# Performance work log

Measured on AMD Instinct MI355X. Metric: run time of the kernel, lower is better.

Reference implementation:

```python
import jax, jax.numpy as jnp
import numpy as np

RADIUS = (0.1, 0.1, 0.1)  # radius_x, radius_y, radius_z (cube half-widths)
NSAMPLE = 32


def setup_inputs() -> dict:
    key = jax.random.key(0)
    k1, k2, k3 = jax.random.split(key, 3)
    B, Nb, Mb, C = 4, 16384, 4096, 64
    xyz = jax.random.uniform(k1, (B * Nb, 3), dtype=jnp.float32)
    new_xyz = jax.random.uniform(k2, (B * Mb, 3), dtype=jnp.float32)
    features = jax.random.normal(k3, (B * Nb, C), dtype=jnp.float32)
    xyz_batch_cnt = jnp.full((B,), Nb, dtype=jnp.int32)
    new_xyz_batch_cnt = jnp.full((B,), Mb, dtype=jnp.int32)
    return {
        "xyz": xyz,
        "xyz_batch_cnt": xyz_batch_cnt,
        "new_xyz": new_xyz,
        "new_xyz_batch_cnt": new_xyz_batch_cnt,
        "features": features,
    }


def _cube_query(xyz_b, new_b, rx, ry, rz, nsample):
    # xyz_b: (B, Nb, 3); new_b: (B, Mb, 3)
    Nb = xyz_b.shape[1]

    def per_batch(args):
        pts, qs = args  # (Nb,3), (Mb,3)
        # cube membership test per axis (avoid stacking a (Mb,Nb,3) tensor)
        mask = (
            (jnp.abs(qs[:, None, 0] - pts[None, :, 0]) < rx)
            & (jnp.abs(qs[:, None, 1] - pts[None, :, 1]) < ry)
            & (jnp.abs(qs[:, None, 2] - pts[None, :, 2]) < rz)
        )  # (Mb, Nb)
        # CUDA kernel keeps the FIRST nsample neighbors in point order:
        # score favors in-cube points, tie-broken by smallest index.
        score = jnp.where(mask, -jnp.arange(Nb, dtype=jnp.float32), -jnp.inf)
        vals, idx_local = jax.lax.top_k(score, nsample)  # (Mb, nsample)
        valid = jnp.isfinite(vals)  # non_padding
        return idx_local, valid

    # process one batch at a time to bound the MbxNb intermediate
    idx_l, valid = jax.lax.map(per_batch, (xyz_b, new_b))
    return idx_l, valid


def reference(xyz, xyz_batch_cnt, new_xyz, new_xyz_batch_cnt, features):
    rx, ry, rz = RADIUS
    nsample = NSAMPLE
    B = xyz_batch_cnt.shape[0]
    N, M = xyz.shape[0], new_xyz.shape[0]
    Nb, Mb = N // B, M // B  # equal counts per batch (matches setup_inputs)

    xyz_b = xyz.reshape(B, Nb, 3)
    new_b = new_xyz.reshape(B, Mb, 3)

    idx_l, valid = _cube_query(xyz_b, new_b, rx, ry, rz, nsample)
    # local -> global flattened indices (batch offsets)
    offsets = (jnp.arange(B, dtype=idx_l.dtype) * Nb)[:, None, None]
    idx = (idx_l + offsets).reshape(M, nsample)
    valid = valid.reshape(M, nsample)
    # torch zeroes idx for empty/padding slots before gather
    idx = jnp.where(valid, idx, 0)

    non_padding = valid.astype(features.dtype)  # (M, nsample)
    grouped = features[idx]  # (M, nsample, C) gather
    # empty_ball_mask + padding_mask zeroing, fused into one multiply
    grouped = grouped * non_padding[..., None]
    grouped = jnp.transpose(grouped, (0, 2, 1))  # (M, C, nsample)
    num_non_padding = jnp.sum(non_padding, axis=-1)  # (M,)
    return grouped, num_non_padding
```

## Files before the change

kernel.cpp:

```cpp
#include <hip/hip_runtime.h>

#define NSAMPLE 32
#define RADI 0.1f
#define WPB 4
#define MARGIN 0.0002f

#define NCELL 4
#define NBLKA 3
#define SPAN  2
#define NBLK3 27
#define CAP   3072
#define NSEG  64

typedef float nat_f32x4 __attribute__((ext_vector_type(4)));

__device__ __forceinline__ int cell_of(float x) {
    int c = (int)(x * (float)NCELL);
    c = c < 0 ? 0 : c;
    return c > (NCELL - 1) ? (NCELL - 1) : c;
}

__global__ __launch_bounds__(256) void pack_xyz_kernel(
    const float* __restrict__ xyz, float4* __restrict__ xyz4, int N)
{
    const int i = blockIdx.x * blockDim.x + threadIdx.x;
    if (i < N) {
        float4 v;
        v.x = xyz[i * 3 + 0];
        v.y = xyz[i * 3 + 1];
        v.z = xyz[i * 3 + 2];
        v.w = 0.0f;
        xyz4[i] = v;
    }
}

__global__ __launch_bounds__(64 * WPB) void count_kernel(
    const float4* __restrict__ xyz4, const int* __restrict__ xyz_cnt,
    int* __restrict__ segcnt, int B)
{
    const int wave = threadIdx.x >> 6, lane = threadIdx.x & 63;
    const int gw = blockIdx.x * WPB + wave;
    if (gw >= B * NBLK3 * NSEG) return;
    const int seg = gw % NSEG;
    const int blk = (gw / NSEG) % NBLK3;
    const int b   = gw / (NSEG * NBLK3);
    const int bx = blk % NBLKA, by = (blk / NBLKA) % NBLKA, bz = blk / (NBLKA * NBLKA);

    int xstart = 0;
    for (int i = 0; i < b; ++i) xstart += xyz_cnt[i];
    const int nb = xyz_cnt[b];
    const int seglen = (nb + NSEG - 1) / NSEG;
    const int p0 = seg * seglen;
    const int p1 = min(p0 + seglen, nb);

    int cnt = 0;
    for (int base = p0; base < p1; base += 256) {
        #pragma unroll
        for (int k = 0; k < 4; ++k) {
            const int p = base + k * 64 + lane;
            bool hit = false;
            if (p < p1) {
                const float4 v = xyz4[xstart + p];
                hit = ((unsigned)(cell_of(v.x) - bx) < (unsigned)SPAN) &
                      ((unsigned)(cell_of(v.y) - by) < (unsigned)SPAN) &
                      ((unsigned)(cell_of(v.z) - bz) < (unsigned)SPAN);
            }
            cnt += (int)__popcll(__ballot(hit));
        }
    }
    if (lane == 0) segcnt[gw] = cnt;
}

__global__ __launch_bounds__(64 * WPB) void fill_kernel(
    const float4* __restrict__ xyz4, const int* __restrict__ xyz_cnt,
    const int* __restrict__ segcnt, float4* __restrict__ blk_pts,
    int* __restrict__ blkcnt, int B)
{
    const int wave = threadIdx.x >> 6, lane = threadIdx.x & 63;
    const int gw = blockIdx.x * WPB + wave;
    if (gw >= B * NBLK3 * NSEG) return;
    const int seg = gw % NSEG;
    const int blk = (gw / NSEG) % NBLK3;
    const int b   = gw / (NSEG * NBLK3);
    const int bx = blk % NBLKA, by = (blk / NBLKA) % NBLKA, bz = blk / (NBLKA * NBLKA);

    int xstart = 0;
    for (int i = 0; i < b; ++i) xstart += xyz_cnt[i];
    const int nb = xyz_cnt[b];
    const int seglen = (nb + NSEG - 1) / NSEG;
    const int p0 = seg * seglen;
    const int p1 = min(p0 + seglen, nb);

    const int bid = b * NBLK3 + blk;
    int off = 0;
    const int sbase = bid * NSEG;
    for (int s = 0; s < seg; ++s) off += segcnt[sbase + s];

    float4* __restrict__ dst = blk_pts + (size_t)bid * CAP;
    const unsigned long long lt = (1ull << lane) - 1ull;

    int cnt = 0;
    for (int base = p0; base < p1; base += 256) {
        #pragma unroll
        for (int k = 0; k < 4; ++k) {
            const int p = base + k * 64 + lane;
            bool hit = false;
            float4 v;
            if (p < p1) {
                v = xyz4[xstart + p];
                hit = ((unsigned)(cell_of(v.x) - bx) < (unsigned)SPAN) &
                      ((unsigned)(cell_of(v.y) - by) < (unsigned)SPAN) &
                      ((unsigned)(cell_of(v.z) - bz) < (unsigned)SPAN);
            }
            const unsigned long long m = __ballot(hit);
            if (hit) {
                const int slot = off + cnt + (int)__popcll(m & lt);
                if (slot < CAP) {
                    v.w = __int_as_float(xstart + p);
                    dst[slot] = v;
                }
            }
            cnt += (int)__popcll(m);
        }
    }
    if (seg == NSEG - 1 && lane == 0) blkcnt[bid] = off + cnt;
}

__global__ __launch_bounds__(64 * WPB, 8) void query_kernel(
    const float4* __restrict__ blk_pts,
    const int*    __restrict__ blkcnt,
    const float*  __restrict__ new_xyz,
    const int*    __restrict__ new_cnt,
    const float*  __restrict__ features,
    float* __restrict__ out_grouped,
    float* __restrict__ out_cnt,
    int B, int M, int C)
{
    const int wave = threadIdx.x >> 6;
    const int lane = threadIdx.x & 63;
    const int q = blockIdx.x * WPB + wave;
    if (q >= M) return;

    __shared__ int s_idx_all[WPB][NSAMPLE];
    int* __restrict__ s_idx = s_idx_all[wave];
    if (lane < NSAMPLE) s_idx[lane] = 0;

    int b = 0, qacc = 0;
    for (int i = 0; i < B; ++i) {
        const int qc = new_cnt[i];
        if (q < qacc + qc) { b = i; break; }
        qacc += qc;
    }

    const float qx = new_xyz[q * 3 + 0];
    const float qy = new_xyz[q * 3 + 1];
    const float qz = new_xyz[q * 3 + 2];

    const int bxq = min(max((int)floorf((qx - RADI - MARGIN) * (float)NCELL), 0), NBLKA - 1);
    const int byq = min(max((int)floorf((qy - RADI - MARGIN) * (float)NCELL), 0), NBLKA - 1);
    const int bzq = min(max((int)floorf((qz - RADI - MARGIN) * (float)NCELL), 0), NBLKA - 1);
    const int bid = b * NBLK3 + bxq + NBLKA * byq + NBLKA * NBLKA * bzq;

    int lcnt = blkcnt[bid];
    if (lcnt > CAP) lcnt = CAP;

    const float4* __restrict__ lp = blk_pts + (size_t)bid * CAP;
    const unsigned long long lt = (1ull << lane) - 1ull;

    int found = 0, base = 0;
    const int nfull = lcnt & ~255;

    auto test_group = [&](const float4& v, bool inb) {
        const float m3 = fmaxf(fmaxf(fabsf(qx - v.x), fabsf(qy - v.y)),
                               fabsf(qz - v.z));
        const bool c = inb & (m3 < RADI);
        const unsigned long long m = __ballot(c);
        if (c) {
            const int slot = found + (int)__popcll(m & lt);
            if (slot < NSAMPLE) s_idx[slot] = __float_as_int(v.w);
        }
        found += (int)__popcll(m);
    };

    if (nfull > 0) {
        float4 A[4], Bb[4];
        #pragma unroll
        for (int k = 0; k < 4; ++k) A[k] = lp[k * 64 + lane];

        while (true) {
            int nxt = base + 256;
            if (nxt < nfull) {
                #pragma unroll
                for (int k = 0; k < 4; ++k) Bb[k] = lp[nxt + k * 64 + lane];
            }
            #pragma unroll
            for (int k = 0; k < 4; ++k) {
                test_group(A[k], true);
                if (found >= NSAMPLE) break;
            }
            base = nxt;
            if (found >= NSAMPLE || base >= nfull) break;

            nxt = base + 256;
            if (nxt < nfull) {
                #pragma unroll
                for (int k = 0; k < 4; ++k) A[k] = lp[nxt + k * 64 + lane];
            }
            #pragma unroll
            for (int k = 0; k < 4; ++k) {
                test_group(Bb[k], true);
                if (found >= NSAMPLE) break;
            }
            base = nxt;
            if (found >= NSAMPLE || base >= nfull) break;
        }
    }
    while (found < NSAMPLE && base < lcnt) {
        #pragma unroll
        for (int k = 0; k < 4; ++k) {
            const int p = base + k * 64 + lane;
            const bool inb = (p < lcnt);
            const float4 v = lp[inb ? p : 0];
            test_group(v, inb);
        }
        base += 256;
    }
    if (found > NSAMPLE) found = NSAMPLE;

    asm volatile("s_waitcnt lgkmcnt(0)" ::: "memory");
    __builtin_amdgcn_sched_barrier(0);

    const int s0  = 4 * (lane & 7);
    const int chi = lane >> 3;
    const int r0 = s_idx[s0 + 0];
    const int r1 = s_idx[s0 + 1];
    const int r2 = s_idx[s0 + 2];
    const int r3 = s_idx[s0 + 3];
    const float k0 = (s0 + 0) < found ? 1.0f : 0.0f;
    const float k1 = (s0 + 1) < found ? 1.0f : 0.0f;
    const float k2 = (s0 + 2) < found ? 1.0f : 0.0f;
    const float k3 = (s0 + 3) < found ? 1.0f : 0.0f;

    const float* __restrict__ f0p = features + (size_t)r0 * C;
    const float* __restrict__ f1p = features + (size_t)r1 * C;
    const float* __restrict__ f2p = features + (size_t)r2 * C;
    const float* __restrict__ f3p = features + (size_t)r3 * C;

    float* __restrict__ og = out_grouped + (size_t)q * (C * NSAMPLE);
    #pragma unroll
    for (int k = 0; k < 8; ++k) {
        const int c = 8 * k + chi;
        nat_f32x4 v;
        v.x = f0p[c] * k0;
        v.y = f1p[c] * k1;
        v.z = f2p[c] * k2;
        v.w = f3p[c] * k3;
        __builtin_nontemporal_store(v,
            reinterpret_cast<nat_f32x4*>(og + (size_t)(k * 64 + lane) * 4));
    }
    if (lane == 0) out_cnt[q] = (float)found;
}

__global__ __launch_bounds__(64 * WPB, 8) void fallback_kernel(
    const float* __restrict__ xyz, const int* __restrict__ xyz_cnt,
    const float* __restrict__ new_xyz, const int* __restrict__ new_cnt,
    const float* __restrict__ features,
    float* __restrict__ out_grouped, float* __restrict__ out_cnt,
    int B, int M, int C)
{
    const int wave = threadIdx.x >> 6, lane = threadIdx.x & 63;
    const int q = blockIdx.x * WPB + wave;
    if (q >= M) return;

    __shared__ int s_idx_all[WPB][NSAMPLE];
    int* __restrict__ s_idx = s_idx_all[wave];
    if (lane < NSAMPLE) s_idx[lane] = 0;

    int b = 0, qacc = 0, xstart = 0;
    for (int i = 0; i < B; ++i) {
        const int qc = new_cnt[i];
        if (q < qacc + qc) { b = i; break; }
        qacc += qc; xstart += xyz_cnt[i];
    }
    const int nb = xyz_cnt[b];
    const float qx = new_xyz[q * 3 + 0], qy = new_xyz[q * 3 + 1], qz = new_xyz[q * 3 + 2];
    const float* __restrict__ xp = xyz + (size_t)xstart * 3;
    const unsigned long long lt = (1ull << lane) - 1ull;

    int found = 0;
    for (int base = 0; base < nb && found < NSAMPLE; base += 64) {
        const int p = base + lane;
        bool c = false;
        if (p < nb) {
            const float dx = qx - xp[p * 3 + 0];
            const float dy = qy - xp[p * 3 + 1];
            const float dz = qz - xp[p * 3 + 2];
            c = (fabsf(dx) < RADI) && (fabsf(dy) < RADI) && (fabsf(dz) < RADI);
        }
        const unsigned long long m = __ballot(c);
        if (c) {
            const int slot = found + (int)__popcll(m & lt);
            if (slot < NSAMPLE) s_idx[slot] = xstart + p;
        }
        found += (int)__popcll(m);
    }
    if (found > NSAMPLE) found = NSAMPLE;

    asm volatile("s_waitcnt lgkmcnt(0)" ::: "memory");
    __builtin_amdgcn_sched_barrier(0);

    const int s0 = 4 * (lane & 7), chi = lane >> 3;
    const int r0 = s_idx[s0 + 0], r1 = s_idx[s0 + 1], r2 = s_idx[s0 + 2], r3 = s_idx[s0 + 3];
    const float k0 = (s0 + 0) < found ? 1.0f : 0.0f;
    const float k1 = (s0 + 1) < found ? 1.0f : 0.0f;
    const float k2 = (s0 + 2) < found ? 1.0f : 0.0f;
    const float k3 = (s0 + 3) < found ? 1.0f : 0.0f;
    const float* f0p = features + (size_t)r0 * C;
    const float* f1p = features + (size_t)r1 * C;
    const float* f2p = features + (size_t)r2 * C;
    const float* f3p = features + (size_t)r3 * C;
    float* __restrict__ og = out_grouped + (size_t)q * (C * NSAMPLE);
    #pragma unroll
    for (int k = 0; k < 8; ++k) {
        const int c = 8 * k + chi;
        float4 v;
        v.x = f0p[c] * k0; v.y = f1p[c] * k1; v.z = f2p[c] * k2; v.w = f3p[c] * k3;
        *reinterpret_cast<float4*>(og + (size_t)(k * 64 + lane) * 4) = v;
    }
    if (lane == 0) out_cnt[q] = (float)found;
}

extern "C" void kernel_launch(void* const* d_in, const int* in_sizes, int n_in,
                              void* d_out, int out_size, void* d_ws, size_t ws_size,
                              hipStream_t stream) {
    const float* xyz      = (const float*)d_in[0];
    const int*   xyz_cnt  = (const int*)d_in[1];
    const float* new_xyz  = (const float*)d_in[2];
    const int*   new_cnt  = (const int*)d_in[3];
    const float* features = (const float*)d_in[4];

    const int B = in_sizes[1];
    const int N = in_sizes[0] / 3;
    const int M = in_sizes[2] / 3;
    const int C = in_sizes[4] / N;

    float* out_grouped = (float*)d_out;
    float* out_cnt     = (float*)d_out + (size_t)M * C * NSAMPLE;

    const size_t pack_bytes = (size_t)N * sizeof(float4);
    const size_t blk_bytes  = (size_t)B * NBLK3 * CAP * sizeof(float4);
    const size_t seg_bytes  = (size_t)B * NBLK3 * NSEG * sizeof(int);
    const size_t bcn_bytes  = (size_t)B * NBLK3 * sizeof(int);
    const size_t need = pack_bytes + blk_bytes + seg_bytes + bcn_bytes;

    if (ws_size >= need) {
        float4* xyz4    = (float4*)d_ws;
        float4* blk_pts = (float4*)((char*)d_ws + pack_bytes);
        int*    segcnt  = (int*)((char*)d_ws + pack_bytes + blk_bytes);
        int*    blkcnt  = (int*)((char*)d_ws + pack_bytes + blk_bytes + seg_bytes);

        hipLaunchKernelGGL(pack_xyz_kernel, dim3((N + 255) / 256), dim3(256), 0, stream,
                           xyz, xyz4, N);
        const int nbw = B * NBLK3 * NSEG;
        hipLaunchKernelGGL(count_kernel, dim3((nbw + WPB - 1) / WPB), dim3(64 * WPB), 0, stream,
                           xyz4, xyz_cnt, segcnt, B);
        hipLaunchKernelGGL(fill_kernel, dim3((nbw + WPB - 1) / WPB), dim3(64 * WPB), 0, stream,
                           xyz4, xyz_cnt, segcnt, blk_pts, blkcnt, B);
        hipLaunchKernelGGL(query_kernel, dim3((M + WPB - 1) / WPB), dim3(64 * WPB), 0, stream,
                           blk_pts, blkcnt, new_xyz, new_cnt, features,
                           out_grouped, out_cnt, B, M, C);
    } else {
        hipLaunchKernelGGL(fallback_kernel, dim3((M + WPB - 1) / WPB), dim3(64 * WPB), 0, stream,
                           xyz, xyz_cnt, new_xyz, new_cnt, features,
                           out_grouped, out_cnt, B, M, C);
    }
}
```

Measured before the change: 74.04 us.

## Bucket queries by spatial block so waves in a workgroup share point lists

Adds a bucket kernel that groups query points by their coarse spatial block using atomics, and a templated query kernel that walks these buckets so neighbouring waves scan the same block point list. The goal is better L2/cache reuse of the per-block point arrays and less per-query batch/block computation. The cost is an extra kernel launch plus atomics, and a sparse launch grid of B*27*QCAP slots where many waves exit early. There is also a capacity heuristic with a fallback to the unbucketed path.

```diff
diff --git a/kernel.cpp b/kernel.cpp
--- a/kernel.cpp
+++ b/kernel.cpp
@@ -12,6 +12,9 @@
 #define CAP   3072
 #define NSEG  64
 
+#define QCAP 512
+#define CPAD 32
+
 typedef float nat_f32x4 __attribute__((ext_vector_type(4)));
 
 __device__ __forceinline__ int cell_of(float x) {
@@ -21,9 +24,11 @@
 }
 
 __global__ __launch_bounds__(256) void pack_xyz_kernel(
-    const float* __restrict__ xyz, float4* __restrict__ xyz4, int N)
+    const float* __restrict__ xyz, float4* __restrict__ xyz4,
+    int* __restrict__ bcnt, int N, int B)
 {
     const int i = blockIdx.x * blockDim.x + threadIdx.x;
+    if (i < B * NBLK3 * CPAD) bcnt[i] = 0;
     if (i < N) {
         float4 v;
         v.x = xyz[i * 3 + 0];
@@ -126,9 +131,37 @@
     if (seg == NSEG - 1 && lane == 0) blkcnt[bid] = off + cnt;
 }
 
+__global__ __launch_bounds__(256) void bucket_kernel(
+    const float* __restrict__ new_xyz, const int* __restrict__ new_cnt,
+    int* __restrict__ bcnt, int* __restrict__ qidx, int B, int M)
+{
+    const int q = blockIdx.x * blockDim.x + threadIdx.x;
+    if (q >= M) return;
+
+    int b = 0, qacc = 0;
+    for (int i = 0; i < B; ++i) {
+        const int qc = new_cnt[i];
+        if (q < qacc + qc) { b = i; break; }
+        qacc += qc;
+    }
+    const float qx = new_xyz[q * 3 + 0];
+    const float qy = new_xyz[q * 3 + 1];
+    const float qz = new_xyz[q * 3 + 2];
+    const int bxq = min(max((int)floorf((qx - RADI - MARGIN) * (float)NCELL), 0), NBLKA - 1);
+    const int byq = min(max((int)floorf((qy - RADI - MARGIN) * (float)NCELL), 0), NBLKA - 1);
+    const int bzq = min(max((int)floorf((qz - RADI - MARGIN) * (float)NCELL), 0), NBLKA - 1);
+    const int bid = b * NBLK3 + bxq + NBLKA * byq + NBLKA * NBLKA * bzq;
+
+    const int pos = atomicAdd(&bcnt[bid * CPAD], 1);
+    if (pos < QCAP) qidx[bid * QCAP + pos] = q;
+}
+
+template <bool BUCKETED>
 __global__ __launch_bounds__(64 * WPB, 8) void query_kernel(
     const float4* __restrict__ blk_pts,
     const int*    __restrict__ blkcnt,
+    const int*    __restrict__ bcnt,
+    const int*    __restrict__ qidx,
     const float*  __restrict__ new_xyz,
     const int*    __restrict__ new_cnt,
     const float*  __restrict__ features,
@@ -138,28 +171,42 @@
 {
     const int wave = threadIdx.x >> 6;
     const int lane = threadIdx.x & 63;
-    const int q = blockIdx.x * WPB + wave;
-    if (q >= M) return;
+    const int gw = blockIdx.x * WPB + wave;
 
     __shared__ int s_idx_all[WPB][NSAMPLE];
     int* __restrict__ s_idx = s_idx_all[wave];
+
+    int q, bid;
+    if (BUCKETED) {
+        bid = gw / QCAP;
+        const int pos = gw % QCAP;
+        int bq = bcnt[bid * CPAD];
+        if (bq > QCAP) bq = QCAP;
+        if (pos >= bq) return;
+        q = qidx[bid * QCAP + pos];
+    } else {
+        q = gw;
+        if (q >= M) return;
+    }
+
     if (lane < NSAMPLE) s_idx[lane] = 0;
-
-    int b = 0, qacc = 0;
-    for (int i = 0; i < B; ++i) {
-        const int qc = new_cnt[i];
-        if (q < qacc + qc) { b = i; break; }
-        qacc += qc;
-    }
 
     const float qx = new_xyz[q * 3 + 0];
     const float qy = new_xyz[q * 3 + 1];
     const float qz = new_xyz[q * 3 + 2];
 
-    const int bxq = min(max((int)floorf((qx - RADI - MARGIN) * (float)NCELL), 0), NBLKA - 1);
-    const int byq = min(max((int)floorf((qy - RADI - MARGIN) * (float)NCELL), 0), NBLKA - 1);
-    const int bzq = min(max((int)floorf((qz - RADI - MARGIN) * (float)NCELL), 0), NBLKA - 1);
-    const int bid = b * NBLK3 + bxq + NBLKA * byq + NBLKA * NBLKA * bzq;
+    if (!BUCKETED) {
+        int b = 0, qacc = 0;
+        for (int i = 0; i < B; ++i) {
+            const int qc = new_cnt[i];
+            if (q < qacc + qc) { b = i; break; }
+            qacc += qc;
+        }
+        const int bxq = min(max((int)floorf((qx - RADI - MARGIN) * (float)NCELL), 0), NBLKA - 1);
+        const int byq = min(max((int)floorf((qy - RADI - MARGIN) * (float)NCELL), 0), NBLKA - 1);
+        const int bzq = min(max((int)floorf((qz - RADI - MARGIN) * (float)NCELL), 0), NBLKA - 1);
+        bid = b * NBLK3 + bxq + NBLKA * byq + NBLKA * NBLKA * bzq;
+    }
 
     int lcnt = blkcnt[bid];
     if (lcnt > CAP) lcnt = CAP;
@@ -351,24 +398,48 @@
     const size_t blk_bytes  = (size_t)B * NBLK3 * CAP * sizeof(float4);
     const size_t seg_bytes  = (size_t)B * NBLK3 * NSEG * sizeof(int);
     const size_t bcn_bytes  = (size_t)B * NBLK3 * sizeof(int);
-    const size_t need = pack_bytes + blk_bytes + seg_bytes + bcn_bytes;
-
-    if (ws_size >= need) {
-        float4* xyz4    = (float4*)d_ws;
-        float4* blk_pts = (float4*)((char*)d_ws + pack_bytes);
-        int*    segcnt  = (int*)((char*)d_ws + pack_bytes + blk_bytes);
-        int*    blkcnt  = (int*)((char*)d_ws + pack_bytes + blk_bytes + seg_bytes);
+    const size_t buc_bytes  = (size_t)B * NBLK3 * CPAD * sizeof(int);
+    const size_t qix_bytes  = (size_t)B * NBLK3 * QCAP * sizeof(int);
+
+    const size_t need_bucketed = pack_bytes + blk_bytes + seg_bytes + bcn_bytes
+                               + buc_bytes + qix_bytes;
+    const size_t need_basic    = pack_bytes + blk_bytes + seg_bytes + bcn_bytes + buc_bytes;
+
+    double mb = (B > 0 ? (double)M / B : (double)M) * 0.064;
+    const bool cap_ok = (mb + 6.0 * __builtin_sqrt(mb + 1.0) + 16.0) < (double)QCAP;
+
+    if (ws_size >= need_basic) {
+        char* w = (char*)d_ws;
+        float4* xyz4    = (float4*)w;                       w += pack_bytes;
+        float4* blk_pts = (float4*)w;                       w += blk_bytes;
+        int*    segcnt  = (int*)w;                          w += seg_bytes;
+        int*    blkcnt  = (int*)w;                          w += bcn_bytes;
+        int*    bcnt    = (int*)w;                          w += buc_bytes;
+        int*    qidx    = (int*)w;
+
+        const bool bucketed = cap_ok && (ws_size >= need_bucketed);
 
         hipLaunchKernelGGL(pack_xyz_kernel, dim3((N + 255) / 256), dim3(256), 0, stream,
-                           xyz, xyz4, N);
+                           xyz, xyz4, bcnt, N, B);
         const int nbw = B * NBLK3 * NSEG;
         hipLaunchKernelGGL(count_kernel, dim3((nbw + WPB - 1) / WPB), dim3(64 * WPB), 0, stream,
                            xyz4, xyz_cnt, segcnt, B);
         hipLaunchKernelGGL(fill_kernel, dim3((nbw + WPB - 1) / WPB), dim3(64 * WPB), 0, stream,
                            xyz4, xyz_cnt, segcnt, blk_pts, blkcnt, B);
-        hipLaunchKernelGGL(query_kernel, dim3((M + WPB - 1) / WPB), dim3(64 * WPB), 0, stream,
-                           blk_pts, blkcnt, new_xyz, new_cnt, features,
-                           out_grouped, out_cnt, B, M, C);
+        if (bucketed) {
+            hipLaunchKernelGGL(bucket_kernel, dim3((M + 255) / 256), dim3(256), 0, stream,
+                               new_xyz, new_cnt, bcnt, qidx, B, M);
+            const int nslots = B * NBLK3 * QCAP;
+            hipLaunchKernelGGL((query_kernel<true>), dim3((nslots + WPB - 1) / WPB),
+                               dim3(64 * WPB), 0, stream,
+                               blk_pts, blkcnt, bcnt, qidx, new_xyz, new_cnt, features,
+                               out_grouped, out_cnt, B, M, C);
+        } else {
+            hipLaunchKernelGGL((query_kernel<false>), dim3((M + WPB - 1) / WPB),
+                               dim3(64 * WPB), 0, stream,
+                               blk_pts, blkcnt, bcnt, qidx, new_xyz, new_cnt, features,
+                               out_grouped, out_cnt, B, M, C);
+        }
     } else {
         hipLaunchKernelGGL(fallback_kernel, dim3((M + WPB - 1) / WPB), dim3(64 * WPB), 0, stream,
                            xyz, xyz_cnt, new_xyz, new_cnt, features,
```

Result: slower. 95.22 us (+28.6%).

## Process two queries per wavefront with interleaved scan streams

Applied to the files above, without the earlier changes.

Each wavefront now handles two query points and interleaves their neighbor scans, so two independent load/ballot chains can overlap and hide latency. The per-iteration batch shrinks from four to two groups of 64 points per query, double-buffered. Occupancy hint lowered from 8 to 6 to allow more registers, and the grid is halved. The risk is fewer waves overall, plus divergence when the two queries finish at different times.

```diff
diff --git a/kernel.cpp b/kernel.cpp
--- a/kernel.cpp
+++ b/kernel.cpp
@@ -126,7 +126,7 @@
     if (seg == NSEG - 1 && lane == 0) blkcnt[bid] = off + cnt;
 }
 
-__global__ __launch_bounds__(64 * WPB, 8) void query_kernel(
+__global__ __launch_bounds__(64 * WPB, 6) void query_kernel(
     const float4* __restrict__ blk_pts,
     const int*    __restrict__ blkcnt,
     const float*  __restrict__ new_xyz,
@@ -138,127 +138,175 @@
 {
     const int wave = threadIdx.x >> 6;
     const int lane = threadIdx.x & 63;
-    const int q = blockIdx.x * WPB + wave;
-    if (q >= M) return;
-
-    __shared__ int s_idx_all[WPB][NSAMPLE];
-    int* __restrict__ s_idx = s_idx_all[wave];
-    if (lane < NSAMPLE) s_idx[lane] = 0;
-
-    int b = 0, qacc = 0;
-    for (int i = 0; i < B; ++i) {
-        const int qc = new_cnt[i];
-        if (q < qacc + qc) { b = i; break; }
-        qacc += qc;
-    }
-
-    const float qx = new_xyz[q * 3 + 0];
-    const float qy = new_xyz[q * 3 + 1];
-    const float qz = new_xyz[q * 3 + 2];
-
-    const int bxq = min(max((int)floorf((qx - RADI - MARGIN) * (float)NCELL), 0), NBLKA - 1);
-    const int byq = min(max((int)floorf((qy - RADI - MARGIN) * (float)NCELL), 0), NBLKA - 1);
-    const int bzq = min(max((int)floorf((qz - RADI - MARGIN) * (float)NCELL), 0), NBLKA - 1);
-    const int bid = b * NBLK3 + bxq + NBLKA * byq + NBLKA * NBLKA * bzq;
-
-    int lcnt = blkcnt[bid];
-    if (lcnt > CAP) lcnt = CAP;
-
-    const float4* __restrict__ lp = blk_pts + (size_t)bid * CAP;
+    const int q0 = (blockIdx.x * WPB + wave) * 2;
+    if (q0 >= M) return;
+    const int q1 = q0 + 1;
+    const bool has1 = q1 < M;
+
+    __shared__ int s_idx_all[WPB][2][NSAMPLE];
+    int* __restrict__ sp0 = s_idx_all[wave][0];
+    int* __restrict__ sp1 = s_idx_all[wave][1];
+    (&s_idx_all[wave][0][0])[lane] = 0;
+
+    float qx0, qy0, qz0, qx1, qy1, qz1;
+    int bid0, bid1;
+    {
+        int b = 0, qacc = 0;
+        for (int i = 0; i < B; ++i) {
+            const int qc = new_cnt[i];
+            if (q0 < qacc + qc) { b = i; break; }
+            qacc += qc;
+        }
+        qx0 = new_xyz[q0 * 3 + 0]; qy0 = new_xyz[q0 * 3 + 1]; qz0 = new_xyz[q0 * 3 + 2];
+        const int bx = min(max((int)floorf((qx0 - RADI - MARGIN) * (float)NCELL), 0), NBLKA - 1);
+        const int by = min(max((int)floorf((qy0 - RADI - MARGIN) * (float)NCELL), 0), NBLKA - 1);
+        const int bz = min(max((int)floorf((qz0 - RADI - MARGIN) * (float)NCELL), 0), NBLKA - 1);
+        bid0 = b * NBLK3 + bx + NBLKA * by + NBLKA * NBLKA * bz;
+    }
+    if (has1) {
+        int b = 0, qacc = 0;
+        for (int i = 0; i < B; ++i) {
+            const int qc = new_cnt[i];
+            if (q1 < qacc + qc) { b = i; break; }
+            qacc += qc;
+        }
+        qx1 = new_xyz[q1 * 3 + 0]; qy1 = new_xyz[q1 * 3 + 1]; qz1 = new_xyz[q1 * 3 + 2];
+        const int bx = min(max((int)floorf((qx1 - RADI - MARGIN) * (float)NCELL), 0), NBLKA - 1);
+        const int by = min(max((int)floorf((qy1 - RADI - MARGIN) * (float)NCELL), 0), NBLKA - 1);
+        const int bz = min(max((int)floorf((qz1 - RADI - MARGIN) * (float)NCELL), 0), NBLKA - 1);
+        bid1 = b * NBLK3 + bx + NBLKA * by + NBLKA * NBLKA * bz;
+    } else {
+        qx1 = qx0; qy1 = qy0; qz1 = qz0; bid1 = bid0;
+    }
+
+    int lcnt0 = blkcnt[bid0]; if (lcnt0 > CAP) lcnt0 = CAP;
+    int lcnt1 = has1 ? blkcnt[bid1] : 0; if (lcnt1 > CAP) lcnt1 = CAP;
+
+    const float4* __restrict__ lp0 = blk_pts + (size_t)bid0 * CAP;
+    const float4* __restrict__ lp1 = blk_pts + (size_t)bid1 * CAP;
     const unsigned long long lt = (1ull << lane) - 1ull;
 
-    int found = 0, base = 0;
-    const int nfull = lcnt & ~255;
-
-    auto test_group = [&](const float4& v, bool inb) {
+    int f0 = 0, f1 = 0, base0 = 0, base1 = 0;
+    bool act0 = (lcnt0 > 0);
+    bool act1 = has1 && (lcnt1 > 0);
+
+    auto tst = [&](const float4& v, float qx, float qy, float qz,
+                   int* __restrict__ sp, int& fnd, bool inb) {
         const float m3 = fmaxf(fmaxf(fabsf(qx - v.x), fabsf(qy - v.y)),
                                fabsf(qz - v.z));
         const bool c = inb & (m3 < RADI);
         const unsigned long long m = __ballot(c);
         if (c) {
-            const int slot = found + (int)__popcll(m & lt);
-            if (slot < NSAMPLE) s_idx[slot] = __float_as_int(v.w);
-        }
-        found += (int)__popcll(m);
+            const int slot = fnd + (int)__popcll(m & lt);
+            if (slot < NSAMPLE) sp[slot] = __float_as_int(v.w);
+        }
+        fnd += (int)__popcll(m);
     };
 
-    if (nfull > 0) {
-        float4 A[4], Bb[4];
-        #pragma unroll
-        for (int k = 0; k < 4; ++k) A[k] = lp[k * 64 + lane];
-
-        while (true) {
-            int nxt = base + 256;
-            if (nxt < nfull) {
-                #pragma unroll
-                for (int k = 0; k < 4; ++k) Bb[k] = lp[nxt + k * 64 + lane];
-            }
-            #pragma unroll
-            for (int k = 0; k < 4; ++k) {
-                test_group(A[k], true);
-                if (found >= NSAMPLE) break;
-            }
-            base = nxt;
-            if (found >= NSAMPLE || base >= nfull) break;
-
-            nxt = base + 256;
-            if (nxt < nfull) {
-                #pragma unroll
-                for (int k = 0; k < 4; ++k) A[k] = lp[nxt + k * 64 + lane];
-            }
-            #pragma unroll
-            for (int k = 0; k < 4; ++k) {
-                test_group(Bb[k], true);
-                if (found >= NSAMPLE) break;
-            }
-            base = nxt;
-            if (found >= NSAMPLE || base >= nfull) break;
-        }
-    }
-    while (found < NSAMPLE && base < lcnt) {
-        #pragma unroll
-        for (int k = 0; k < 4; ++k) {
-            const int p = base + k * 64 + lane;
-            const bool inb = (p < lcnt);
-            const float4 v = lp[inb ? p : 0];
-            test_group(v, inb);
-        }
-        base += 256;
-    }
-    if (found > NSAMPLE) found = NSAMPLE;
+    float4 A0[2], Bv0[2], A1[2], Bv1[2];
+    if (act0) { A0[0] = lp0[lane]; A0[1] = lp0[64 + lane]; }
+    if (act1) { A1[0] = lp1[lane]; A1[1] = lp1[64 + lane]; }
+
+    while (act0 | act1) {
+        if (act0 && (base0 + 128 < lcnt0)) {
+            Bv0[0] = lp0[base0 + 128 + lane]; Bv0[1] = lp0[base0 + 192 + lane];
+        }
+        if (act1 && (base1 + 128 < lcnt1)) {
+            Bv1[0] = lp1[base1 + 128 + lane]; Bv1[1] = lp1[base1 + 192 + lane];
+        }
+        if (act0) {
+            tst(A0[0], qx0, qy0, qz0, sp0, f0, base0 + lane < lcnt0);
+            tst(A0[1], qx0, qy0, qz0, sp0, f0, base0 + 64 + lane < lcnt0);
+            base0 += 128;
+            act0 = (f0 < NSAMPLE) & (base0 < lcnt0);
+        }
+        if (act1) {
+            tst(A1[0], qx1, qy1, qz1, sp1, f1, base1 + lane < lcnt1);
+            tst(A1[1], qx1, qy1, qz1, sp1, f1, base1 + 64 + lane < lcnt1);
+            base1 += 128;
+            act1 = (f1 < NSAMPLE) & (base1 < lcnt1);
+        }
+        if (!(act0 | act1)) break;
+
+        if (act0 && (base0 + 128 < lcnt0)) {
+            A0[0] = lp0[base0 + 128 + lane]; A0[1] = lp0[base0 + 192 + lane];
+        }
+        if (act1 && (base1 + 128 < lcnt1)) {
+            A1[0] = lp1[base1 + 128 + lane]; A1[1] = lp1[base1 + 192 + lane];
+        }
+        if (act0) {
+            tst(Bv0[0], qx0, qy0, qz0, sp0, f0, base0 + lane < lcnt0);
+            tst(Bv0[1], qx0, qy0, qz0, sp0, f0, base0 + 64 + lane < lcnt0);
+            base0 += 128;
+            act0 = (f0 < NSAMPLE) & (base0 < lcnt0);
+        }
+        if (act1) {
+            tst(Bv1[0], qx1, qy1, qz1, sp1, f1, base1 + lane < lcnt1);
+            tst(Bv1[1], qx1, qy1, qz1, sp1, f1, base1 + 64 + lane < lcnt1);
+            base1 += 128;
+            act1 = (f1 < NSAMPLE) & (base1 < lcnt1);
+        }
+    }
+    if (f0 > NSAMPLE) f0 = NSAMPLE;
+    if (f1 > NSAMPLE) f1 = NSAMPLE;
 
     asm volatile("s_waitcnt lgkmcnt(0)" ::: "memory");
     __builtin_amdgcn_sched_barrier(0);
 
     const int s0  = 4 * (lane & 7);
     const int chi = lane >> 3;
-    const int r0 = s_idx[s0 + 0];
-    const int r1 = s_idx[s0 + 1];
-    const int r2 = s_idx[s0 + 2];
-    const int r3 = s_idx[s0 + 3];
-    const float k0 = (s0 + 0) < found ? 1.0f : 0.0f;
-    const float k1 = (s0 + 1) < found ? 1.0f : 0.0f;
-    const float k2 = (s0 + 2) < found ? 1.0f : 0.0f;
-    const float k3 = (s0 + 3) < found ? 1.0f : 0.0f;
-
-    const float* __restrict__ f0p = features + (size_t)r0 * C;
-    const float* __restrict__ f1p = features + (size_t)r1 * C;
-    const float* __restrict__ f2p = features + (size_t)r2 * C;
-    const float* __restrict__ f3p = features + (size_t)r3 * C;
-
-    float* __restrict__ og = out_grouped + (size_t)q * (C * NSAMPLE);
-    #pragma unroll
-    for (int k = 0; k < 8; ++k) {
-        const int c = 8 * k + chi;
-        nat_f32x4 v;
-        v.x = f0p[c] * k0;
-        v.y = f1p[c] * k1;
-        v.z = f2p[c] * k2;
-        v.w = f3p[c] * k3;
-        __builtin_nontemporal_store(v,
-            reinterpret_cast<nat_f32x4*>(og + (size_t)(k * 64 + lane) * 4));
-    }
-    if (lane == 0) out_cnt[q] = (float)found;
+    {
+        const int r0 = sp0[s0 + 0], r1 = sp0[s0 + 1];
+        const int r2 = sp0[s0 + 2], r3 = sp0[s0 + 3];
+        const float k0 = (s0 + 0) < f0 ? 1.0f : 0.0f;
+        const float k1 = (s0 + 1) < f0 ? 1.0f : 0.0f;
+        const float k2 = (s0 + 2) < f0 ? 1.0f : 0.0f;
+        const float k3 = (s0 + 3) < f0 ? 1.0f : 0.0f;
+        const float* __restrict__ f0p = features + (size_t)r0 * C;
+        const float* __restrict__ f1p = features + (size_t)r1 * C;
+        const float* __restrict__ f2p = features + (size_t)r2 * C;
+        const float* __restrict__ f3p = features + (size_t)r3 * C;
+        float* __restrict__ og = out_grouped + (size_t)q0 * (C * NSAMPLE);
+        #pragma unroll
+        for (int k = 0; k < 8; ++k) {
+            const int c = 8 * k + chi;
+            nat_f32x4 v;
+            v.x = f0p[c] * k0;
+            v.y = f1p[c] * k1;
+            v.z = f2p[c] * k2;
+            v.w = f3p[c] * k3;
+            __builtin_nontemporal_store(v,
+                reinterpret_cast<nat_f32x4*>(og + (size_t)(k * 64 + lane) * 4));
+        }
+    }
+    if (has1) {
+        const int r0 = sp1[s0 + 0], r1 = sp1[s0 + 1];
+        const int r2 = sp1[s0 + 2], r3 = sp1[s0 + 3];
+        const float k0 = (s0 + 0) < f1 ? 1.0f : 0.0f;
+        const float k1 = (s0 + 1) < f1 ? 1.0f : 0.0f;
+        const float k2 = (s0 + 2) < f1 ? 1.0f : 0.0f;
+        const float k3 = (s0 + 3) < f1 ? 1.0f : 0.0f;
+        const float* __restrict__ f0p = features + (size_t)r0 * C;
+        const float* __restrict__ f1p = features + (size_t)r1 * C;
+        const float* __restrict__ f2p = features + (size_t)r2 * C;
+        const float* __restrict__ f3p = features + (size_t)r3 * C;
+        float* __restrict__ og = out_grouped + (size_t)q1 * (C * NSAMPLE);
+        #pragma unroll
+        for (int k = 0; k < 8; ++k) {
+            const int c = 8 * k + chi;
+            nat_f32x4 v;
+            v.x = f0p[c] * k0;
+            v.y = f1p[c] * k1;
+            v.z = f2p[c] * k2;
+            v.w = f3p[c] * k3;
+            __builtin_nontemporal_store(v,
+                reinterpret_cast<nat_f32x4*>(og + (size_t)(k * 64 + lane) * 4));
+        }
+    }
+    if (lane == 0) {
+        out_cnt[q0] = (float)f0;
+        if (has1) out_cnt[q1] = (float)f1;
+    }
 }
 
 __global__ __launch_bounds__(64 * WPB, 8) void fallback_kernel(
@@ -354,10 +402,11 @@
     const size_t need = pack_bytes + blk_bytes + seg_bytes + bcn_bytes;
 
     if (ws_size >= need) {
-        float4* xyz4    = (float4*)d_ws;
-        float4* blk_pts = (float4*)((char*)d_ws + pack_bytes);
-        int*    segcnt  = (int*)((char*)d_ws + pack_bytes + blk_bytes);
-        int*    blkcnt  = (int*)((char*)d_ws + pack_bytes + blk_bytes + seg_bytes);
+        char* w = (char*)d_ws;
+        float4* xyz4    = (float4*)w;                       w += pack_bytes;
+        float4* blk_pts = (float4*)w;                       w += blk_bytes;
+        int*    segcnt  = (int*)w;                          w += seg_bytes;
+        int*    blkcnt  = (int*)w;
 
         hipLaunchKernelGGL(pack_xyz_kernel, dim3((N + 255) / 256), dim3(256), 0, stream,
                            xyz, xyz4, N);
@@ -366,7 +415,8 @@
                            xyz4, xyz_cnt, segcnt, B);
         hipLaunchKernelGGL(fill_kernel, dim3((nbw + WPB - 1) / WPB), dim3(64 * WPB), 0, stream,
                            xyz4, xyz_cnt, segcnt, blk_pts, blkcnt, B);
-        hipLaunchKernelGGL(query_kernel, dim3((M + WPB - 1) / WPB), dim3(64 * WPB), 0, stream,
+        const int pairs = (M + 1) / 2;
+        hipLaunchKernelGGL(query_kernel, dim3((pairs + WPB - 1) / WPB), dim3(64 * WPB), 0, stream,
                            blk_pts, blkcnt, new_xyz, new_cnt, features,
                            out_grouped, out_cnt, B, M, C);
     } else {
```

After: 77.59 us. 4.8% more time.
